# Kernel optimization log

Hardware: AMD Instinct MI355X
Metric: run time of the kernel (lower is better)

## Reference

```python
import jax, jax.numpy as jnp
import numpy as np

N, E, F_IN, H, G, C = 50000, 800000, 128, 128, 64, 10
EPS = 1e-5


def _glorot_lin(key, fin, fout):
    s = 1.0 / np.sqrt(fin)
    return jax.random.uniform(key, (fin, fout), jnp.float32, -s, s)


def setup_inputs() -> dict:
    key = jax.random.key(0)
    ks = jax.random.split(key, 24)
    x = jax.random.normal(ks[0], (N, F_IN), jnp.float32)
    edge_index = jax.random.randint(ks[1], (2, E), 0, N)
    batch = jnp.sort(jax.random.randint(ks[2], (N,), 0, G))
    inp = {"x": x, "edge_index": edge_index, "batch": batch}
    # GCNConv weights [in, out] and biases
    dims = [(F_IN, H), (H, H), (H, H), (H, H)]
    for i, (fi, fo) in enumerate(dims, start=1):
        inp[f"W{i}"] = _glorot_lin(ks[2 + i], fi, fo)
        inp[f"b{i}"] = jnp.zeros((fo,), jnp.float32)
    # BatchNorm affine params
    for i in range(1, 4):
        inp[f"g{i}"] = jnp.ones((H,), jnp.float32)
        inp[f"be{i}"] = jnp.zeros((H,), jnp.float32)
    # MLP head
    inp["lw1"] = _glorot_lin(ks[10], 2 * H, H)
    inp["lb1"] = jnp.zeros((H,), jnp.float32)
    inp["lw2"] = _glorot_lin(ks[11], H, C)
    inp["lb2"] = jnp.zeros((C,), jnp.float32)
    return inp


def _gcn_conv(h_in, W, b, src, dst, norm_e, self_norm):
    # linear transform then symmetric-normalized aggregation (incl. self loops)
    h = h_in @ W                                            # [N, out]
    agg = jax.ops.segment_sum(h[src] * norm_e[:, None], dst, num_segments=N)
    return agg + h * self_norm[:, None] + b


def _batch_norm(x, gamma, beta):
    mu = jnp.mean(x, axis=0)
    var = jnp.var(x, axis=0)
    return (x - mu) * jax.lax.rsqrt(var + EPS) * gamma + beta


def reference(x, edge_index, batch, W1, b1, W2, b2, W3, b3, W4, b4,
              g1, be1, g2, be2, g3, be3, lw1, lb1, lw2, lb2):
    src, dst = edge_index[0], edge_index[1]
    # degrees with self loops; GCN symmetric normalization
    deg = jax.ops.segment_sum(jnp.ones((E,), jnp.float32), dst, num_segments=N) + 1.0
    dinv = jax.lax.rsqrt(deg)
    norm_e = dinv[src] * dinv[dst]   # per-edge norm
    self_norm = 1.0 / deg            # self-loop norm = dinv*dinv

    h = jax.nn.relu(_batch_norm(_gcn_conv(x, W1, b1, src, dst, norm_e, self_norm), g1, be1))
    h = jax.nn.relu(_batch_norm(_gcn_conv(h, W2, b2, src, dst, norm_e, self_norm), g2, be2))
    h = jax.nn.relu(_batch_norm(_gcn_conv(h, W3, b3, src, dst, norm_e, self_norm), g3, be3))
    h = jax.nn.relu(_gcn_conv(h, W4, b4, src, dst, norm_e, self_norm))

    counts = jax.ops.segment_sum(jnp.ones((N,), jnp.float32), batch, num_segments=G)
    x_mean = jax.ops.segment_sum(h, batch, num_segments=G) / counts[:, None]
    x_max = jax.ops.segment_max(h, batch, num_segments=G)
    z = jnp.concatenate([x_mean, x_max], axis=1)            # [G, 2H]

    z = jax.nn.relu(z @ lw1 + lb1)
    # dropout is identity in eval mode
    return z @ lw2 + lb2                                    # [G, C]
```

## Files before the change

kernel.cpp:

```cpp
#include <hip/hip_runtime.h>

#define N_NODES 50000
#define N_EDGES 800000
#define HID     128
#define NGRAPH  64
#define BN_EPS  1e-5f
#define SCAN_B  98

__global__ __launch_bounds__(256) void deg_counti_kernel(const int* __restrict__ ei,
                                                         int* __restrict__ degi) {
    int i = blockIdx.x * 256 + threadIdx.x;
    if (i < N_EDGES) atomicAdd(&degi[ei[N_EDGES + i]], 1);
}

__global__ __launch_bounds__(256) void deg_fin_kernel(const int* __restrict__ degi,
                                                      float* __restrict__ dinv) {
    int i = blockIdx.x * 256 + threadIdx.x;
    if (i < N_NODES) dinv[i] = rsqrtf((float)degi[i] + 1.0f);
}

__global__ __launch_bounds__(512) void scan1_kernel(const int* __restrict__ degi,
                                                    int* __restrict__ row_start,
                                                    int* __restrict__ partials) {
    __shared__ int sh[512];
    const int t = threadIdx.x;
    const int i = blockIdx.x * 512 + t;
    const int v = (i < N_NODES) ? degi[i] : 0;
    sh[t] = v;
    __syncthreads();
#pragma unroll
    for (int off = 1; off < 512; off <<= 1) {
        const int add = (t >= off) ? sh[t - off] : 0;
        __syncthreads();
        sh[t] += add;
        __syncthreads();
    }
    if (i < N_NODES) row_start[i] = sh[t] - v;
    if (t == 511) partials[blockIdx.x] = sh[511];
}

__global__ __launch_bounds__(128) void scan2_kernel(int* __restrict__ partials,
                                                    int* __restrict__ row_start) {
    __shared__ int sh[SCAN_B + 1];
    const int t = threadIdx.x;
    if (t < SCAN_B) sh[t] = partials[t];
    __syncthreads();
    if (t == 0) {
        int run = 0;
        for (int b = 0; b < SCAN_B; ++b) { const int v = sh[b]; sh[b] = run; run += v; }
        sh[SCAN_B] = run;
    }
    __syncthreads();
    if (t < SCAN_B) partials[t] = sh[t];
    if (t == 0) row_start[N_NODES] = sh[SCAN_B];
}

__global__ __launch_bounds__(512) void scan3_kernel(int* __restrict__ row_start,
                                                    const int* __restrict__ partials) {
    const int i = blockIdx.x * 512 + threadIdx.x;
    if (i < N_NODES) row_start[i] += partials[blockIdx.x];
}

__global__ __launch_bounds__(256) void scatter_kernel(const int* __restrict__ ei,
                                                      const float* __restrict__ dinv,
                                                      const int* __restrict__ row_start,
                                                      int* __restrict__ cursor,
                                                      float2* __restrict__ csr_sw) {
    int e = blockIdx.x * 256 + threadIdx.x;
    if (e >= N_EDGES) return;
    const int src = ei[e];
    const int dst = ei[N_EDGES + e];
    const int pos = row_start[dst] + atomicAdd(&cursor[dst], 1);
    float2 sw;
    sw.x = __int_as_float(src);
    sw.y = dinv[src] * dinv[dst];
    csr_sw[pos] = sw;
}

__global__ __launch_bounds__(256) void bounds_kernel(const int* __restrict__ batch,
                                                     int* __restrict__ bound) {
    int i = blockIdx.x * 256 + threadIdx.x;
    if (i >= N_NODES) return;
    const int b = batch[i];
    if (i == 0) {
        for (int g = 0; g <= b; ++g) bound[g] = 0;
    } else {
        const int pb = batch[i - 1];
        for (int g = pb + 1; g <= b; ++g) bound[g] = i;
    }
    if (i == N_NODES - 1) {
        for (int g = b + 1; g <= NGRAPH; ++g) bound[g] = N_NODES;
    }
}

__global__ __launch_bounds__(256) void gemm_kernel(const float* __restrict__ X,
                                                   const float* __restrict__ W,
                                                   const float* __restrict__ stats,
                                                   const int use_bn,
                                                   float* __restrict__ hout) {
    __shared__ float xs[64][128];
    __shared__ float wsm[32][128];
    const int tid = threadIdx.x;
    const int block_row = blockIdx.x * 64;

    {
        const float4* Xv = (const float4*)(X + (size_t)block_row * HID);
        float4* xsv = (float4*)&xs[0][0];
        int rows_valid = N_NODES - block_row;
        if (rows_valid > 64) rows_valid = 64;
        const int max4 = rows_valid * 32;
        for (int i = tid; i < 64 * 32; i += 256) {
            float4 v = (i < max4) ? Xv[i] : make_float4(0.f, 0.f, 0.f, 0.f);
            if (use_bn) {
                const int c4 = (i & 31) * 4;
                const float4 sc = *(const float4*)(stats + c4);
                const float4 sh = *(const float4*)(stats + HID + c4);
                v.x = fmaxf(fmaf(v.x, sc.x, sh.x), 0.f);
                v.y = fmaxf(fmaf(v.y, sc.y, sh.y), 0.f);
                v.z = fmaxf(fmaf(v.z, sc.z, sh.z), 0.f);
                v.w = fmaxf(fmaf(v.w, sc.w, sh.w), 0.f);
            }
            xsv[i] = v;
        }
    }

    const int cg = (tid & 31) * 4;
    const int r0 = (tid >> 5) * 8;

    float acc[8][4];
#pragma unroll
    for (int r = 0; r < 8; ++r)
#pragma unroll
        for (int j = 0; j < 4; ++j) acc[r][j] = 0.f;

    for (int kc = 0; kc < 4; ++kc) {
        __syncthreads();
        {
            const float4* Wv = (const float4*)(W + kc * 32 * HID);
            float4* wsv = (float4*)&wsm[0][0];
            for (int i = tid; i < 32 * 32; i += 256) wsv[i] = Wv[i];
        }
        __syncthreads();
#pragma unroll
        for (int kk = 0; kk < 32; ++kk) {
            const float4 w4 = *(const float4*)(&wsm[kk][cg]);
            const int k = kc * 32 + kk;
#pragma unroll
            for (int r = 0; r < 8; ++r) {
                const float xv = xs[r0 + r][k];
                acc[r][0] = fmaf(xv, w4.x, acc[r][0]);
                acc[r][1] = fmaf(xv, w4.y, acc[r][1]);
                acc[r][2] = fmaf(xv, w4.z, acc[r][2]);
                acc[r][3] = fmaf(xv, w4.w, acc[r][3]);
            }
        }
    }

#pragma unroll
    for (int r = 0; r < 8; ++r) {
        const int row = block_row + r0 + r;
        if (row < N_NODES)
            *(float4*)(hout + (size_t)row * HID + cg) =
                make_float4(acc[r][0], acc[r][1], acc[r][2], acc[r][3]);
    }
}

__global__ __launch_bounds__(256) void agg_csr_kernel(const int* __restrict__ row_start,
                                                      const float2* __restrict__ csr_sw,
                                                      const float* __restrict__ h,
                                                      const float* __restrict__ dinv,
                                                      const float* __restrict__ bias,
                                                      float* __restrict__ agg) {
    const int node = blockIdx.x * 4 + (threadIdx.x >> 6);
    if (node >= N_NODES) return;
    const int lane = threadIdx.x & 63;
    const int c = lane * 2;
    const int beg = row_start[node];
    const int end = row_start[node + 1];

    const float dv = dinv[node];
    const float sn = dv * dv;
    const float2 hv = *(const float2*)(h + (size_t)node * HID + c);
    const float2 bv = *(const float2*)(bias + c);
    float2 a0 = make_float2(fmaf(hv.x, sn, bv.x), fmaf(hv.y, sn, bv.y));
    float2 a1 = make_float2(0.f, 0.f);
    float2 a2 = make_float2(0.f, 0.f);
    float2 a3 = make_float2(0.f, 0.f);

    int p = beg;
    for (; p + 4 <= end; p += 4) {
        const float2 e0 = csr_sw[p];
        const float2 e1 = csr_sw[p + 1];
        const float2 e2 = csr_sw[p + 2];
        const float2 e3 = csr_sw[p + 3];
        const float2 v0 = *(const float2*)(h + (size_t)__float_as_int(e0.x) * HID + c);
        const float2 v1 = *(const float2*)(h + (size_t)__float_as_int(e1.x) * HID + c);
        const float2 v2 = *(const float2*)(h + (size_t)__float_as_int(e2.x) * HID + c);
        const float2 v3 = *(const float2*)(h + (size_t)__float_as_int(e3.x) * HID + c);
        a0.x = fmaf(v0.x, e0.y, a0.x); a0.y = fmaf(v0.y, e0.y, a0.y);
        a1.x = fmaf(v1.x, e1.y, a1.x); a1.y = fmaf(v1.y, e1.y, a1.y);
        a2.x = fmaf(v2.x, e2.y, a2.x); a2.y = fmaf(v2.y, e2.y, a2.y);
        a3.x = fmaf(v3.x, e3.y, a3.x); a3.y = fmaf(v3.y, e3.y, a3.y);
    }
    for (; p < end; ++p) {
        const float2 e0 = csr_sw[p];
        const float2 v0 = *(const float2*)(h + (size_t)__float_as_int(e0.x) * HID + c);
        a0.x = fmaf(v0.x, e0.y, a0.x); a0.y = fmaf(v0.y, e0.y, a0.y);
    }
    a0.x += (a1.x + a2.x) + a3.x;
    a0.y += (a1.y + a2.y) + a3.y;
    *(float2*)(agg + (size_t)node * HID + c) = a0;
}

__global__ __launch_bounds__(256) void bn_stats_kernel(const float* __restrict__ a,
                                                       float* __restrict__ stats) {
    const int c = threadIdx.x & 127;
    const int half = threadIdx.x >> 7;
    const int row0 = blockIdx.x * 128;
    int rend = row0 + 128;
    if (rend > N_NODES) rend = N_NODES;
    float s = 0.f, sq = 0.f;
    for (int r = row0 + half; r < rend; r += 2) {
        const float v = a[(size_t)r * HID + c];
        s += v;
        sq = fmaf(v, v, sq);
    }
    __shared__ float sh[2][2][128];
    sh[0][half][c] = s;
    sh[1][half][c] = sq;
    __syncthreads();
    if (half == 0) {
        atomicAdd(&stats[c], sh[0][0][c] + sh[0][1][c]);
        atomicAdd(&stats[HID + c], sh[1][0][c] + sh[1][1][c]);
    }
}

__global__ __launch_bounds__(128) void bn_fin_kernel(float* __restrict__ stats,
                                                     const float* __restrict__ gamma,
                                                     const float* __restrict__ beta) {
    const int c = threadIdx.x;
    const float invN = 1.0f / (float)N_NODES;
    const float mu = stats[c] * invN;
    const float var = stats[HID + c] * invN - mu * mu;
    const float scale = rsqrtf(var + BN_EPS) * gamma[c];
    stats[c] = scale;
    stats[HID + c] = fmaf(-mu, scale, beta[c]);
}

__global__ __launch_bounds__(256) void pool_seg_kernel(const float* __restrict__ a,
                                                       const int* __restrict__ bound,
                                                       float* __restrict__ z) {
    const int g = blockIdx.x;
    const int cl = threadIdx.x & 31;
    const int c = blockIdx.y * 32 + cl;
    const int par = threadIdx.x >> 5;
    const int beg = bound[g], end = bound[g + 1];
    float s = 0.f, m = 0.f;
    for (int r = beg + par; r < end; r += 8) {
        const float v = fmaxf(a[(size_t)r * HID + c], 0.f);
        s += v;
        m = fmaxf(m, v);
    }
    __shared__ float ssum[8][32];
    __shared__ float smax[8][32];
    ssum[par][cl] = s;
    smax[par][cl] = m;
    __syncthreads();
    if (par == 0) {
        float ts = 0.f, tm = 0.f;
#pragma unroll
        for (int p = 0; p < 8; ++p) { ts += ssum[p][cl]; tm = fmaxf(tm, smax[p][cl]); }
        const float cntf = (float)(end - beg);
        z[g * 256 + c] = ts / fmaxf(cntf, 1.f);
        z[g * 256 + 128 + c] = tm;
    }
}

__global__ __launch_bounds__(128) void head_kernel(const float* __restrict__ z,
                                                   const float* __restrict__ lw1,
                                                   const float* __restrict__ lb1,
                                                   const float* __restrict__ lw2,
                                                   const float* __restrict__ lb2,
                                                   float* __restrict__ out) {
    __shared__ float zin[256];
    __shared__ float z1[128];
    const int g = blockIdx.x;
    const int t = threadIdx.x;
    zin[t] = z[g * 256 + t];
    zin[128 + t] = z[g * 256 + 128 + t];
    __syncthreads();
    float accv = lb1[t];
#pragma unroll 4
    for (int k = 0; k < 256; ++k) accv = fmaf(zin[k], lw1[k * 128 + t], accv);
    z1[t] = fmaxf(accv, 0.f);
    __syncthreads();
    if (t < 10) {
        float o = lb2[t];
#pragma unroll 4
        for (int k = 0; k < 128; ++k) o = fmaf(z1[k], lw2[k * 10 + t], o);
        out[g * 10 + t] = o;
    }
}

extern "C" void kernel_launch(void* const* d_in, const int* in_sizes, int n_in,
                              void* d_out, int out_size, void* d_ws, size_t ws_size,
                              hipStream_t stream) {
    const float* x     = (const float*)d_in[0];
    const int*   ei    = (const int*)d_in[1];
    const int*   batch = (const int*)d_in[2];
    const float* W[4]  = {(const float*)d_in[3], (const float*)d_in[5],
                          (const float*)d_in[7], (const float*)d_in[9]};
    const float* B[4]  = {(const float*)d_in[4], (const float*)d_in[6],
                          (const float*)d_in[8], (const float*)d_in[10]};
    const float* Gm[3] = {(const float*)d_in[11], (const float*)d_in[13],
                          (const float*)d_in[15]};
    const float* Be[3] = {(const float*)d_in[12], (const float*)d_in[14],
                          (const float*)d_in[16]};
    const float* lw1 = (const float*)d_in[17];
    const float* lb1 = (const float*)d_in[18];
    const float* lw2 = (const float*)d_in[19];
    const float* lb2 = (const float*)d_in[20];

    char* ws = (char*)d_ws;
    float*  dinv      = (float*)ws;
    float*  stats     = (float*)(ws + 50000u * 4);
    float*  z         = (float*)(ws + 50256u * 4);
    int*    degi      = (int*)  (ws + 66640u * 4);
    int*    cursor    = (int*)  (ws + 116640u * 4);
    int*    row_start = (int*)  (ws + 166640u * 4);
    int*    bound     = (int*)  (ws + 216644u * 4);
    float2* csr_sw    = (float2*)(ws + 216712u * 4);
    float*  hbuf      = (float*)(ws + 1816712u * 4);
    float*  abuf      = (float*)(ws + 8216712u * 4);
    int*    partials  = (int*)  (ws + 14616712u * 4);

    hipMemsetAsync(degi, 0, 100000u * sizeof(int), stream);
    deg_counti_kernel<<<(N_EDGES + 255) / 256, 256, 0, stream>>>(ei, degi);
    deg_fin_kernel<<<(N_NODES + 255) / 256, 256, 0, stream>>>(degi, dinv);
    scan1_kernel<<<SCAN_B, 512, 0, stream>>>(degi, row_start, partials);
    scan2_kernel<<<1, 128, 0, stream>>>(partials, row_start);
    scan3_kernel<<<SCAN_B, 512, 0, stream>>>(row_start, partials);
    scatter_kernel<<<(N_EDGES + 255) / 256, 256, 0, stream>>>(ei, dinv, row_start,
                                                              cursor, csr_sw);
    bounds_kernel<<<(N_NODES + 255) / 256, 256, 0, stream>>>(batch, bound);

    const float* cur = x;
    for (int l = 0; l < 4; ++l) {
        gemm_kernel<<<(N_NODES + 63) / 64, 256, 0, stream>>>(cur, W[l], stats,
                                                             l > 0 ? 1 : 0, hbuf);
        agg_csr_kernel<<<(N_NODES + 3) / 4, 256, 0, stream>>>(row_start, csr_sw, hbuf,
                                                              dinv, B[l], abuf);
        if (l < 3) {
            hipMemsetAsync(stats, 0, 256 * sizeof(float), stream);
            bn_stats_kernel<<<(N_NODES + 127) / 128, 256, 0, stream>>>(abuf, stats);
            bn_fin_kernel<<<1, 128, 0, stream>>>(stats, Gm[l], Be[l]);
        }
        cur = abuf;
    }

    pool_seg_kernel<<<dim3(NGRAPH, 4), 256, 0, stream>>>(abuf, bound, z);
    head_kernel<<<NGRAPH, 128, 0, stream>>>(z, lw1, lb1, lw2, lb2, (float*)d_out);
}
```

Before: 751.0 us.

## Enlarge GEMM tile to 128x128 with swizzled LDS, fuse BN finalize and dinv

```diff
diff --git a/kernel.cpp b/kernel.cpp
--- a/kernel.cpp
+++ b/kernel.cpp
@@ -13,19 +13,15 @@
     if (i < N_EDGES) atomicAdd(&degi[ei[N_EDGES + i]], 1);
 }
 
-__global__ __launch_bounds__(256) void deg_fin_kernel(const int* __restrict__ degi,
-                                                      float* __restrict__ dinv) {
-    int i = blockIdx.x * 256 + threadIdx.x;
-    if (i < N_NODES) dinv[i] = rsqrtf((float)degi[i] + 1.0f);
-}
-
 __global__ __launch_bounds__(512) void scan1_kernel(const int* __restrict__ degi,
                                                     int* __restrict__ row_start,
-                                                    int* __restrict__ partials) {
+                                                    int* __restrict__ partials,
+                                                    float* __restrict__ dinv) {
     __shared__ int sh[512];
     const int t = threadIdx.x;
     const int i = blockIdx.x * 512 + t;
     const int v = (i < N_NODES) ? degi[i] : 0;
+    if (i < N_NODES) dinv[i] = rsqrtf((float)v + 1.0f);
     sh[t] = v;
     __syncthreads();
 #pragma unroll
@@ -96,42 +92,55 @@
 __global__ __launch_bounds__(256) void gemm_kernel(const float* __restrict__ X,
                                                    const float* __restrict__ W,
                                                    const float* __restrict__ stats,
+                                                   const float* __restrict__ gamma,
+                                                   const float* __restrict__ beta,
                                                    const int use_bn,
                                                    float* __restrict__ hout) {
-    __shared__ float xs[64][128];
+    __shared__ float xs[128][128];
     __shared__ float wsm[32][128];
     const int tid = threadIdx.x;
-    const int block_row = blockIdx.x * 64;
+    const int block_row = blockIdx.x * 128;
+
+    if (use_bn && tid < 128) {
+        const float invN = 1.0f / (float)N_NODES;
+        const float mu = stats[tid] * invN;
+        const float var = stats[128 + tid] * invN - mu * mu;
+        const float sc = rsqrtf(var + BN_EPS) * gamma[tid];
+        wsm[0][tid] = sc;
+        wsm[1][tid] = fmaf(-mu, sc, beta[tid]);
+    }
+    __syncthreads();
 
     {
-        const float4* Xv = (const float4*)(X + (size_t)block_row * HID);
-        float4* xsv = (float4*)&xs[0][0];
         int rows_valid = N_NODES - block_row;
-        if (rows_valid > 64) rows_valid = 64;
-        const int max4 = rows_valid * 32;
-        for (int i = tid; i < 64 * 32; i += 256) {
-            float4 v = (i < max4) ? Xv[i] : make_float4(0.f, 0.f, 0.f, 0.f);
+        if (rows_valid > 128) rows_valid = 128;
+        for (int i = tid; i < 128 * 32; i += 256) {
+            const int r = i >> 5;
+            const int c4 = (i & 31) * 4;
+            float4 v = make_float4(0.f, 0.f, 0.f, 0.f);
+            if (r < rows_valid)
+                v = *(const float4*)(X + (size_t)(block_row + r) * HID + c4);
             if (use_bn) {
-                const int c4 = (i & 31) * 4;
-                const float4 sc = *(const float4*)(stats + c4);
-                const float4 sh = *(const float4*)(stats + HID + c4);
+                const float4 sc = *(const float4*)&wsm[0][c4];
+                const float4 sh = *(const float4*)&wsm[1][c4];
                 v.x = fmaxf(fmaf(v.x, sc.x, sh.x), 0.f);
                 v.y = fmaxf(fmaf(v.y, sc.y, sh.y), 0.f);
                 v.z = fmaxf(fmaf(v.z, sc.z, sh.z), 0.f);
                 v.w = fmaxf(fmaf(v.w, sc.w, sh.w), 0.f);
             }
-            xsv[i] = v;
-        }
-    }
-
-    const int cg = (tid & 31) * 4;
-    const int r0 = (tid >> 5) * 8;
-
-    float acc[8][4];
+            *(float4*)&xs[r][c4 ^ (((r >> 3) & 7) << 2)] = v;
+        }
+    }
+
+    const int cgA = (tid & 15) * 4;
+    const int r0 = (tid >> 4) * 8;
+    const int kxor = ((r0 >> 3) & 7) << 2;
+
+    float acc[8][8];
 #pragma unroll
     for (int r = 0; r < 8; ++r)
 #pragma unroll
-        for (int j = 0; j < 4; ++j) acc[r][j] = 0.f;
+        for (int j = 0; j < 8; ++j) acc[r][j] = 0.f;
 
     for (int kc = 0; kc < 4; ++kc) {
         __syncthreads();
@@ -142,16 +151,27 @@
         }
         __syncthreads();
 #pragma unroll
-        for (int kk = 0; kk < 32; ++kk) {
-            const float4 w4 = *(const float4*)(&wsm[kk][cg]);
-            const int k = kc * 32 + kk;
-#pragma unroll
-            for (int r = 0; r < 8; ++r) {
-                const float xv = xs[r0 + r][k];
-                acc[r][0] = fmaf(xv, w4.x, acc[r][0]);
-                acc[r][1] = fmaf(xv, w4.y, acc[r][1]);
-                acc[r][2] = fmaf(xv, w4.z, acc[r][2]);
-                acc[r][3] = fmaf(xv, w4.w, acc[r][3]);
+        for (int kk4 = 0; kk4 < 32; kk4 += 4) {
+            float4 xv[8];
+#pragma unroll
+            for (int r = 0; r < 8; ++r)
+                xv[r] = *(const float4*)&xs[r0 + r][(kc * 32 + kk4) ^ kxor];
+#pragma unroll
+            for (int dk = 0; dk < 4; ++dk) {
+                const float4 wa = *(const float4*)&wsm[kk4 + dk][cgA];
+                const float4 wb = *(const float4*)&wsm[kk4 + dk][cgA + 64];
+#pragma unroll
+                for (int r = 0; r < 8; ++r) {
+                    const float xvv = ((const float*)&xv[r])[dk];
+                    acc[r][0] = fmaf(xvv, wa.x, acc[r][0]);
+                    acc[r][1] = fmaf(xvv, wa.y, acc[r][1]);
+                    acc[r][2] = fmaf(xvv, wa.z, acc[r][2]);
+                    acc[r][3] = fmaf(xvv, wa.w, acc[r][3]);
+                    acc[r][4] = fmaf(xvv, wb.x, acc[r][4]);
+                    acc[r][5] = fmaf(xvv, wb.y, acc[r][5]);
+                    acc[r][6] = fmaf(xvv, wb.z, acc[r][6]);
+                    acc[r][7] = fmaf(xvv, wb.w, acc[r][7]);
+                }
             }
         }
     }
@@ -159,9 +179,13 @@
 #pragma unroll
     for (int r = 0; r < 8; ++r) {
         const int row = block_row + r0 + r;
-        if (row < N_NODES)
-            *(float4*)(hout + (size_t)row * HID + cg) =
+        if (row < N_NODES) {
+            float* hp = hout + (size_t)row * HID;
+            *(float4*)(hp + cgA) =
                 make_float4(acc[r][0], acc[r][1], acc[r][2], acc[r][3]);
+            *(float4*)(hp + cgA + 64) =
+                make_float4(acc[r][4], acc[r][5], acc[r][6], acc[r][7]);
+        }
     }
 }
 
@@ -233,18 +257,6 @@
         atomicAdd(&stats[c], sh[0][0][c] + sh[0][1][c]);
         atomicAdd(&stats[HID + c], sh[1][0][c] + sh[1][1][c]);
     }
-}
-
-__global__ __launch_bounds__(128) void bn_fin_kernel(float* __restrict__ stats,
-                                                     const float* __restrict__ gamma,
-                                                     const float* __restrict__ beta) {
-    const int c = threadIdx.x;
-    const float invN = 1.0f / (float)N_NODES;
-    const float mu = stats[c] * invN;
-    const float var = stats[HID + c] * invN - mu * mu;
-    const float scale = rsqrtf(var + BN_EPS) * gamma[c];
-    stats[c] = scale;
-    stats[HID + c] = fmaf(-mu, scale, beta[c]);
 }
 
 __global__ __launch_bounds__(256) void pool_seg_kernel(const float* __restrict__ a,
@@ -336,8 +348,7 @@
 
     hipMemsetAsync(degi, 0, 100000u * sizeof(int), stream);
     deg_counti_kernel<<<(N_EDGES + 255) / 256, 256, 0, stream>>>(ei, degi);
-    deg_fin_kernel<<<(N_NODES + 255) / 256, 256, 0, stream>>>(degi, dinv);
-    scan1_kernel<<<SCAN_B, 512, 0, stream>>>(degi, row_start, partials);
+    scan1_kernel<<<SCAN_B, 512, 0, stream>>>(degi, row_start, partials, dinv);
     scan2_kernel<<<1, 128, 0, stream>>>(partials, row_start);
     scan3_kernel<<<SCAN_B, 512, 0, stream>>>(row_start, partials);
     scatter_kernel<<<(N_EDGES + 255) / 256, 256, 0, stream>>>(ei, dinv, row_start,
@@ -346,14 +357,14 @@
 
     const float* cur = x;
     for (int l = 0; l < 4; ++l) {
-        gemm_kernel<<<(N_NODES + 63) / 64, 256, 0, stream>>>(cur, W[l], stats,
-                                                             l > 0 ? 1 : 0, hbuf);
+        gemm_kernel<<<(N_NODES + 127) / 128, 256, 0, stream>>>(
+            cur, W[l], stats, l > 0 ? Gm[l - 1] : Gm[0], l > 0 ? Be[l - 1] : Be[0],
+            l > 0 ? 1 : 0, hbuf);
         agg_csr_kernel<<<(N_NODES + 3) / 4, 256, 0, stream>>>(row_start, csr_sw, hbuf,
                                                               dinv, B[l], abuf);
         if (l < 3) {
             hipMemsetAsync(stats, 0, 256 * sizeof(float), stream);
             bn_stats_kernel<<<(N_NODES + 127) / 128, 256, 0, stream>>>(abuf, stats);
-            bn_fin_kernel<<<1, 128, 0, stream>>>(stats, Gm[l], Be[l]);
         }
         cur = abuf;
     }
```

Result: slower. 787.2 us (+4.8%).
